# Performance work log

Measured on AMD Instinct MI355X. Metric: run time of the kernel, lower is better.

Reference implementation:

```python
import jax, jax.numpy as jnp
import numpy as np

N = 200000  # nodes
C = 256     # per-node feature dim

def setup_inputs() -> dict:
    key = jax.random.key(0)
    k1, k2, k3, k4, k5, k6, k7 = jax.random.split(key, 7)
    out1 = jax.random.normal(k1, (N, C), dtype=jnp.float32)
    out2 = jax.random.normal(k2, (N, C), dtype=jnp.float32)
    neighbour = jax.random.randint(k3, (N, 3), 0, N, dtype=jnp.int64)
    # Combination2: Conv1d(512,512,1) == Linear(512->512)
    W_comb = jax.random.normal(k4, (512, 2 * C), dtype=jnp.float32) * (1.0 / np.sqrt(2 * C))
    b_comb = jax.random.normal(k5, (512,), dtype=jnp.float32) * 0.01
    # Aggregation2: Conv1d(256,512,1) == Linear(256->512)
    W_agg = jax.random.normal(k6, (512, C), dtype=jnp.float32) * (1.0 / np.sqrt(C))
    b_agg = jax.random.normal(k7, (512,), dtype=jnp.float32) * 0.01
    return {"out1": out1, "out2": out2, "neighbour": neighbour,
            "W_comb": W_comb, "b_comb": b_comb, "W_agg": W_agg, "b_agg": b_agg}


def reference(out1, out2, neighbour, W_comb, b_comb, W_agg, b_agg):
    # Combination2: concat features then 1x1 conv (per-node linear)
    a1 = jnp.concatenate([out1, out2], axis=1)              # [N, 512]
    out3 = jnp.einsum('nc,oc->no', a1, W_comb) + b_comb     # [N, 512]

    # Aggregation2: mean of self + 3 gathered neighbors, then linear 256->512
    neigh_feats = jnp.take(out2, neighbour, axis=0)          # [N, 3, C]
    agg = (out2 + neigh_feats.sum(axis=1)) * 0.25            # [N, C]
    out4 = jnp.einsum('nc,oc->no', agg, W_agg) + b_agg       # [N, 512]
    return (out3, out4)
```

## Files before the change

kernel.cpp:

```cpp
#include <hip/hip_runtime.h>


typedef __bf16 bf16x8 __attribute__((ext_vector_type(8)));
typedef float f32x4 __attribute__((ext_vector_type(4)));

#define N_NODES 200000
#define BM 32
#define NTILES (N_NODES / BM)
#define ROWC 520
#define ROWA 264
#define GRID_B 2048

__device__ __forceinline__ unsigned short f2bf(float x) {
  union { float f; unsigned int u; } v; v.f = x;
  return (unsigned short)((v.u + 0x7FFFu + ((v.u >> 16) & 1u)) >> 16);
}

__device__ __forceinline__ void st_bf4(unsigned short* p, float4 f) {
  uint2 w;
  w.x = (unsigned int)f2bf(f.x) | ((unsigned int)f2bf(f.y) << 16);
  w.y = (unsigned int)f2bf(f.z) | ((unsigned int)f2bf(f.w) << 16);
  *reinterpret_cast<uint2*>(p) = w;
}

__global__ void pack_w_kernel(const float* __restrict__ Wc,
                              const float* __restrict__ Wa,
                              unsigned short* __restrict__ Pc,
                              unsigned short* __restrict__ Pa) {
  int t = blockIdx.x * 256 + threadIdx.x;
  if (t >= (512 + 256) * 64) return;
  int lane = t & 63;
  int tile = t >> 6;
  const float* W;
  unsigned short* P;
  int K, kt_n;
  if (tile < 512) { W = Wc; P = Pc; K = 512; kt_n = 16; }
  else { tile -= 512; W = Wa; P = Pa; K = 256; kt_n = 8; }
  int nt = tile / kt_n;
  int kt = tile - nt * kt_n;
  int row = nt * 16 + (lane & 15);
  int k0 = kt * 32 + (lane >> 4) * 8;
  const float* src = W + (size_t)row * K + k0;
  unsigned short* dst = P + (size_t)tile * 512 + lane * 8;
#pragma unroll
  for (int j = 0; j < 8; ++j) dst[j] = f2bf(src[j]);
}

__global__ __launch_bounds__(512, 2) void gemm_kernel(
    const float* __restrict__ out1, const float* __restrict__ out2,
    const unsigned short* __restrict__ Pc, const unsigned short* __restrict__ Pa,
    const float* __restrict__ b_comb,
    float* __restrict__ out3, unsigned short* __restrict__ Y) {
  __shared__ unsigned short Acomb[BM * ROWC];

  const int tid = threadIdx.x;
  const int ln = tid >> 4, c16 = tid & 15;
  const int wave = tid >> 6, lane = tid & 63;
  const int l15 = lane & 15, l4 = lane >> 4;
  const long long node0 = (long long)blockIdx.x * BM;

  {
    const size_t gn = (size_t)node0 + ln;
    const float4* r1 = reinterpret_cast<const float4*>(out1 + gn * 256);
    const float4* r2 = reinterpret_cast<const float4*>(out2 + gn * 256);
#pragma unroll
    for (int r = 0; r < 4; ++r) {
      const int cc = c16 + 16 * r;
      st_bf4(&Acomb[ln * ROWC + cc * 4], r1[cc]);
      st_bf4(&Acomb[ln * ROWC + 256 + cc * 4], r2[cc]);
    }
  }
  __syncthreads();

  const int nt0 = wave * 4;

  {
    f32x4 acc[2][4];
#pragma unroll
    for (int m = 0; m < 2; ++m)
#pragma unroll
      for (int n = 0; n < 4; ++n) acc[m][n] = (f32x4){0.f, 0.f, 0.f, 0.f};

    const unsigned short* pc = Pc + (size_t)nt0 * 16 * 512 + lane * 8;
    const unsigned short* ab = &Acomb[(size_t)l15 * ROWC + l4 * 8];
#pragma unroll
    for (int kt = 0; kt < 16; ++kt) {
      bf16x8 a0 = *reinterpret_cast<const bf16x8*>(ab + kt * 32);
      bf16x8 a1 = *reinterpret_cast<const bf16x8*>(ab + 16 * ROWC + kt * 32);
      bf16x8 bfr[4];
#pragma unroll
      for (int n = 0; n < 4; ++n)
        bfr[n] = *reinterpret_cast<const bf16x8*>(pc + ((size_t)n * 16 + kt) * 512);
#pragma unroll
      for (int n = 0; n < 4; ++n) {
        acc[0][n] = __builtin_amdgcn_mfma_f32_16x16x32_bf16(a0, bfr[n], acc[0][n], 0, 0, 0);
        acc[1][n] = __builtin_amdgcn_mfma_f32_16x16x32_bf16(a1, bfr[n], acc[1][n], 0, 0, 0);
      }
    }
    float* o3 = out3 + node0 * 512 + wave * 64 + l15;
#pragma unroll
    for (int m = 0; m < 2; ++m)
#pragma unroll
      for (int r = 0; r < 4; ++r) {
        float* p = o3 + (long long)(m * 16 + l4 * 4 + r) * 512;
#pragma unroll
        for (int n = 0; n < 4; ++n)
          p[n * 16] = acc[m][n][r] + b_comb[wave * 64 + n * 16 + l15];
      }
  }

  {
    f32x4 acc[2][4];
#pragma unroll
    for (int m = 0; m < 2; ++m)
#pragma unroll
      for (int n = 0; n < 4; ++n) acc[m][n] = (f32x4){0.f, 0.f, 0.f, 0.f};

    const unsigned short* pa = Pa + (size_t)nt0 * 8 * 512 + lane * 8;
    const unsigned short* ab = &Acomb[(size_t)l15 * ROWC + 256 + l4 * 8];
#pragma unroll
    for (int kt = 0; kt < 8; ++kt) {
      bf16x8 a0 = *reinterpret_cast<const bf16x8*>(ab + kt * 32);
      bf16x8 a1 = *reinterpret_cast<const bf16x8*>(ab + 16 * ROWC + kt * 32);
      bf16x8 bfr[4];
#pragma unroll
      for (int n = 0; n < 4; ++n)
        bfr[n] = *reinterpret_cast<const bf16x8*>(pa + ((size_t)n * 8 + kt) * 512);
#pragma unroll
      for (int n = 0; n < 4; ++n) {
        acc[0][n] = __builtin_amdgcn_mfma_f32_16x16x32_bf16(a0, bfr[n], acc[0][n], 0, 0, 0);
        acc[1][n] = __builtin_amdgcn_mfma_f32_16x16x32_bf16(a1, bfr[n], acc[1][n], 0, 0, 0);
      }
    }

    __syncthreads();
#pragma unroll
    for (int m = 0; m < 2; ++m)
#pragma unroll
      for (int r = 0; r < 4; ++r) {
        const int row = m * 16 + l4 * 4 + r;
#pragma unroll
        for (int n = 0; n < 4; ++n)
          Acomb[row * ROWC + wave * 64 + n * 16 + l15] = f2bf(acc[m][n][r]);
      }
    __syncthreads();

    {
      const int row = tid >> 4;
      const unsigned short* src = &Acomb[row * ROWC];
      unsigned short* dst = Y + (node0 + row) * 512;
#pragma unroll
      for (int j = 0; j < 4; ++j) {
        const int off = (c16 + 16 * j) * 8;
        *reinterpret_cast<uint4*>(dst + off) =
            *reinterpret_cast<const uint4*>(src + off);
      }
    }
  }
}

__device__ __forceinline__ float bf_lo(unsigned u) {
  union { unsigned x; float f; } c; c.x = u << 16; return c.f;
}
__device__ __forceinline__ float bf_hi(unsigned u) {
  union { unsigned x; float f; } c; c.x = u & 0xFFFF0000u; return c.f;
}

__global__ __launch_bounds__(256) void gather_kernel(
    const unsigned short* __restrict__ Y, const int* __restrict__ nbr,
    const float* __restrict__ b_agg, float* __restrict__ out4) {
  const int lane = threadIdx.x & 63;
  const int wid = (blockIdx.x * 256 + threadIdx.x) >> 6;
  const int nwaves = (GRID_B * 256) >> 6;

  float ba[8];
  const float* bp = b_agg + lane * 8;
#pragma unroll
  for (int j = 0; j < 8; ++j) ba[j] = bp[j];

  for (int n = wid; n < N_NODES; n += nwaves) {
    int i0 = nbr[3 * n + 0];
    int i1 = nbr[3 * n + 1];
    int i2 = nbr[3 * n + 2];
    i0 = i0 < 0 ? 0 : (i0 >= N_NODES ? N_NODES - 1 : i0);
    i1 = i1 < 0 ? 0 : (i1 >= N_NODES ? N_NODES - 1 : i1);
    i2 = i2 < 0 ? 0 : (i2 >= N_NODES ? N_NODES - 1 : i2);

    const uint4 a  = *reinterpret_cast<const uint4*>(Y + (size_t)n  * 512 + lane * 8);
    const uint4 b0 = *reinterpret_cast<const uint4*>(Y + (size_t)i0 * 512 + lane * 8);
    const uint4 b1 = *reinterpret_cast<const uint4*>(Y + (size_t)i1 * 512 + lane * 8);
    const uint4 b2 = *reinterpret_cast<const uint4*>(Y + (size_t)i2 * 512 + lane * 8);

    const unsigned wa[4] = {a.x, a.y, a.z, a.w};
    const unsigned w0[4] = {b0.x, b0.y, b0.z, b0.w};
    const unsigned w1[4] = {b1.x, b1.y, b1.z, b1.w};
    const unsigned w2[4] = {b2.x, b2.y, b2.z, b2.w};
    float s[8];
#pragma unroll
    for (int w = 0; w < 4; ++w) {
      s[2 * w]     = bf_lo(wa[w]) + bf_lo(w0[w]) + bf_lo(w1[w]) + bf_lo(w2[w]);
      s[2 * w + 1] = bf_hi(wa[w]) + bf_hi(w0[w]) + bf_hi(w1[w]) + bf_hi(w2[w]);
    }
    f32x4 o0 = {s[0] * 0.25f + ba[0], s[1] * 0.25f + ba[1],
                s[2] * 0.25f + ba[2], s[3] * 0.25f + ba[3]};
    f32x4 o1 = {s[4] * 0.25f + ba[4], s[5] * 0.25f + ba[5],
                s[6] * 0.25f + ba[6], s[7] * 0.25f + ba[7]};
    f32x4* op = reinterpret_cast<f32x4*>(out4 + (size_t)n * 512 + lane * 8);
    op[0] = o0;
    op[1] = o1;
  }
}

__global__ __launch_bounds__(512, 4) void mesh_fused_fallback(
    const float* __restrict__ out1, const float* __restrict__ out2,
    const int* __restrict__ nbr,
    const unsigned short* __restrict__ Pc, const unsigned short* __restrict__ Pa,
    const float* __restrict__ b_comb, const float* __restrict__ b_agg,
    float* __restrict__ outp) {
  __shared__ unsigned short Ac[32 * ROWC];
  __shared__ unsigned short Aagg[32 * ROWA];
  const int tid = threadIdx.x;
  const long long node0 = (long long)blockIdx.x * 32;
  {
    const int ln = tid >> 4, c16 = tid & 15;
    const long long gn = node0 + ln;
    long long i0 = nbr[3 * gn + 0], i1 = nbr[3 * gn + 1], i2 = nbr[3 * gn + 2];
    i0 = i0 < 0 ? 0 : (i0 >= N_NODES ? N_NODES - 1 : i0);
    i1 = i1 < 0 ? 0 : (i1 >= N_NODES ? N_NODES - 1 : i1);
    i2 = i2 < 0 ? 0 : (i2 >= N_NODES ? N_NODES - 1 : i2);
    const float4* r1 = reinterpret_cast<const float4*>(out1 + gn * 256);
    const float4* r2 = reinterpret_cast<const float4*>(out2 + gn * 256);
    const float4* g0 = reinterpret_cast<const float4*>(out2 + i0 * 256);
    const float4* g1 = reinterpret_cast<const float4*>(out2 + i1 * 256);
    const float4* g2 = reinterpret_cast<const float4*>(out2 + i2 * 256);
#pragma unroll
    for (int r = 0; r < 4; ++r) {
      const int c = c16 + 16 * r;
      float4 f1 = r1[c], f2 = r2[c], n0 = g0[c], n1 = g1[c], n2 = g2[c];
      float4 ag;
      ag.x = (f2.x + n0.x + n1.x + n2.x) * 0.25f;
      ag.y = (f2.y + n0.y + n1.y + n2.y) * 0.25f;
      ag.z = (f2.z + n0.z + n1.z + n2.z) * 0.25f;
      ag.w = (f2.w + n0.w + n1.w + n2.w) * 0.25f;
      st_bf4(&Ac[ln * ROWC + c * 4], f1);
      st_bf4(&Ac[ln * ROWC + 256 + c * 4], f2);
      st_bf4(&Aagg[ln * ROWA + c * 4], ag);
    }
  }
  __syncthreads();
  const int wave = tid >> 6, lane = tid & 63;
  const int l15 = lane & 15, l4 = lane >> 4;
  const int nt0 = wave * 4;
  float* o3 = outp;
  float* o4 = outp + (size_t)N_NODES * 512;
  {
    f32x4 acc[2][4];
#pragma unroll
    for (int m = 0; m < 2; ++m)
#pragma unroll
      for (int n = 0; n < 4; ++n) acc[m][n] = (f32x4){0.f, 0.f, 0.f, 0.f};
    const unsigned short* pc = Pc + (size_t)nt0 * 16 * 512 + lane * 8;
    const unsigned short* ab = &Ac[(size_t)l15 * ROWC + l4 * 8];
#pragma unroll
    for (int kt = 0; kt < 16; ++kt) {
      bf16x8 a0 = *reinterpret_cast<const bf16x8*>(ab + kt * 32);
      bf16x8 a1 = *reinterpret_cast<const bf16x8*>(ab + 16 * ROWC + kt * 32);
#pragma unroll
      for (int n = 0; n < 4; ++n) {
        bf16x8 b = *reinterpret_cast<const bf16x8*>(pc + ((size_t)n * 16 + kt) * 512);
        acc[0][n] = __builtin_amdgcn_mfma_f32_16x16x32_bf16(a0, b, acc[0][n], 0, 0, 0);
        acc[1][n] = __builtin_amdgcn_mfma_f32_16x16x32_bf16(a1, b, acc[1][n], 0, 0, 0);
      }
    }
#pragma unroll
    for (int m = 0; m < 2; ++m)
#pragma unroll
      for (int r = 0; r < 4; ++r)
#pragma unroll
        for (int n = 0; n < 4; ++n) {
          const int col = wave * 64 + n * 16 + l15;
          o3[(node0 + m * 16 + l4 * 4 + r) * 512 + col] = acc[m][n][r] + b_comb[col];
        }
  }
  {
    f32x4 acc[2][4];
#pragma unroll
    for (int m = 0; m < 2; ++m)
#pragma unroll
      for (int n = 0; n < 4; ++n) acc[m][n] = (f32x4){0.f, 0.f, 0.f, 0.f};
    const unsigned short* pa = Pa + (size_t)nt0 * 8 * 512 + lane * 8;
    const unsigned short* ab = &Aagg[(size_t)l15 * ROWA + l4 * 8];
#pragma unroll
    for (int kt = 0; kt < 8; ++kt) {
      bf16x8 a0 = *reinterpret_cast<const bf16x8*>(ab + kt * 32);
      bf16x8 a1 = *reinterpret_cast<const bf16x8*>(ab + 16 * ROWA + kt * 32);
#pragma unroll
      for (int n = 0; n < 4; ++n) {
        bf16x8 b = *reinterpret_cast<const bf16x8*>(pa + ((size_t)n * 8 + kt) * 512);
        acc[0][n] = __builtin_amdgcn_mfma_f32_16x16x32_bf16(a0, b, acc[0][n], 0, 0, 0);
        acc[1][n] = __builtin_amdgcn_mfma_f32_16x16x32_bf16(a1, b, acc[1][n], 0, 0, 0);
      }
    }
#pragma unroll
    for (int m = 0; m < 2; ++m)
#pragma unroll
      for (int r = 0; r < 4; ++r)
#pragma unroll
        for (int n = 0; n < 4; ++n) {
          const int col = wave * 64 + n * 16 + l15;
          o4[(node0 + m * 16 + l4 * 4 + r) * 512 + col] = acc[m][n][r] + b_agg[col];
        }
  }
}

extern "C" void kernel_launch(void* const* d_in, const int* in_sizes, int n_in,
                              void* d_out, int out_size, void* d_ws, size_t ws_size,
                              hipStream_t stream) {
  const float* out1 = (const float*)d_in[0];
  const float* out2 = (const float*)d_in[1];
  const int* nbr = (const int*)d_in[2];
  const float* Wc = (const float*)d_in[3];
  const float* bc = (const float*)d_in[4];
  const float* Wa = (const float*)d_in[5];
  const float* ba = (const float*)d_in[6];

  const size_t yElems = (size_t)N_NODES * 512;
  const size_t packElems = 512 * 512 + 512 * 256;
  const size_t need = (yElems + packElems) * 2;

  if (ws_size >= need) {
    unsigned short* Yw = (unsigned short*)d_ws;
    unsigned short* Pc = Yw + yElems;
    unsigned short* Pa = Pc + 512 * 512;
    pack_w_kernel<<<192, 256, 0, stream>>>(Wc, Wa, Pc, Pa);
    gemm_kernel<<<NTILES, 512, 0, stream>>>(out1, out2, Pc, Pa, bc, (float*)d_out, Yw);
    gather_kernel<<<GRID_B, 256, 0, stream>>>(Yw, nbr, ba,
                                              (float*)d_out + (size_t)N_NODES * 512);
  } else {
    unsigned short* Pc = (unsigned short*)d_ws;
    unsigned short* Pa = Pc + 512 * 512;
    pack_w_kernel<<<192, 256, 0, stream>>>(Wc, Wa, Pc, Pa);
    mesh_fused_fallback<<<N_NODES / 32, 512, 0, stream>>>(out1, out2, nbr, Pc, Pa, bc, ba,
                                                          (float*)d_out);
  }
}
```

Baseline: 538.9 us.

## Make GEMM kernel persistent with register prefetch of next tile's inputs

The GEMM kernel becomes a persistent grid-stride loop over node tiles (512 blocks). Each iteration issues global loads for the next tile's out1/out2 rows into registers before the MFMA work on the current tile, so load latency overlaps with compute. It also hoists the b_comb bias load out of the loop. The cost is higher register pressure from the prefetch buffers, plus a fixed grid that may underfill the device or leave tiles unevenly spread across blocks.

```diff
diff --git a/kernel.cpp b/kernel.cpp
--- a/kernel.cpp
+++ b/kernel.cpp
@@ -9,6 +9,7 @@
 #define NTILES (N_NODES / BM)
 #define ROWC 520
 #define ROWA 264
+#define GRID_A 512
 #define GRID_B 2048
 
 __device__ __forceinline__ unsigned short f2bf(float x) {
@@ -57,105 +58,127 @@
   const int ln = tid >> 4, c16 = tid & 15;
   const int wave = tid >> 6, lane = tid & 63;
   const int l15 = lane & 15, l4 = lane >> 4;
-  const long long node0 = (long long)blockIdx.x * BM;
-
-  {
-    const size_t gn = (size_t)node0 + ln;
+  const int nt0 = wave * 4;
+
+  float bcv[4];
+#pragma unroll
+  for (int n = 0; n < 4; ++n) bcv[n] = b_comb[wave * 64 + n * 16 + l15];
+
+  float4 s1[4], s2[4];
+  auto issue = [&](int t) {
+    const size_t gn = (size_t)t * BM + ln;
     const float4* r1 = reinterpret_cast<const float4*>(out1 + gn * 256);
     const float4* r2 = reinterpret_cast<const float4*>(out2 + gn * 256);
 #pragma unroll
     for (int r = 0; r < 4; ++r) {
+      s1[r] = r1[c16 + 16 * r];
+      s2[r] = r2[c16 + 16 * r];
+    }
+  };
+
+  int t = blockIdx.x;
+  issue(t);
+  while (t < NTILES) {
+    __builtin_amdgcn_s_barrier();
+
+#pragma unroll
+    for (int r = 0; r < 4; ++r) {
       const int cc = c16 + 16 * r;
-      st_bf4(&Acomb[ln * ROWC + cc * 4], r1[cc]);
-      st_bf4(&Acomb[ln * ROWC + 256 + cc * 4], r2[cc]);
-    }
-  }
-  __syncthreads();
-
-  const int nt0 = wave * 4;
-
-  {
-    f32x4 acc[2][4];
-#pragma unroll
-    for (int m = 0; m < 2; ++m)
-#pragma unroll
-      for (int n = 0; n < 4; ++n) acc[m][n] = (f32x4){0.f, 0.f, 0.f, 0.f};
-
-    const unsigned short* pc = Pc + (size_t)nt0 * 16 * 512 + lane * 8;
-    const unsigned short* ab = &Acomb[(size_t)l15 * ROWC + l4 * 8];
-#pragma unroll
-    for (int kt = 0; kt < 16; ++kt) {
-      bf16x8 a0 = *reinterpret_cast<const bf16x8*>(ab + kt * 32);
-      bf16x8 a1 = *reinterpret_cast<const bf16x8*>(ab + 16 * ROWC + kt * 32);
-      bf16x8 bfr[4];
-#pragma unroll
-      for (int n = 0; n < 4; ++n)
-        bfr[n] = *reinterpret_cast<const bf16x8*>(pc + ((size_t)n * 16 + kt) * 512);
-#pragma unroll
-      for (int n = 0; n < 4; ++n) {
-        acc[0][n] = __builtin_amdgcn_mfma_f32_16x16x32_bf16(a0, bfr[n], acc[0][n], 0, 0, 0);
-        acc[1][n] = __builtin_amdgcn_mfma_f32_16x16x32_bf16(a1, bfr[n], acc[1][n], 0, 0, 0);
-      }
-    }
-    float* o3 = out3 + node0 * 512 + wave * 64 + l15;
-#pragma unroll
-    for (int m = 0; m < 2; ++m)
-#pragma unroll
-      for (int r = 0; r < 4; ++r) {
-        float* p = o3 + (long long)(m * 16 + l4 * 4 + r) * 512;
+      st_bf4(&Acomb[ln * ROWC + cc * 4], s1[r]);
+      st_bf4(&Acomb[ln * ROWC + 256 + cc * 4], s2[r]);
+    }
+
+    const int tn = t + GRID_A;
+    if (tn < NTILES) issue(tn);
+
+    asm volatile("s_waitcnt lgkmcnt(0)" ::: "memory");
+    __builtin_amdgcn_s_barrier();
+
+    const long long node0 = (long long)t * BM;
+
+    {
+      f32x4 acc[2][4];
+#pragma unroll
+      for (int m = 0; m < 2; ++m)
+#pragma unroll
+        for (int n = 0; n < 4; ++n) acc[m][n] = (f32x4){0.f, 0.f, 0.f, 0.f};
+
+      const unsigned short* pc = Pc + (size_t)nt0 * 16 * 512 + lane * 8;
+      const unsigned short* ab = &Acomb[(size_t)l15 * ROWC + l4 * 8];
+#pragma unroll
+      for (int kt = 0; kt < 16; ++kt) {
+        bf16x8 a0 = *reinterpret_cast<const bf16x8*>(ab + kt * 32);
+        bf16x8 a1 = *reinterpret_cast<const bf16x8*>(ab + 16 * ROWC + kt * 32);
+        bf16x8 bfr[4];
 #pragma unroll
         for (int n = 0; n < 4; ++n)
-          p[n * 16] = acc[m][n][r] + b_comb[wave * 64 + n * 16 + l15];
-      }
-  }
-
-  {
-    f32x4 acc[2][4];
-#pragma unroll
-    for (int m = 0; m < 2; ++m)
-#pragma unroll
-      for (int n = 0; n < 4; ++n) acc[m][n] = (f32x4){0.f, 0.f, 0.f, 0.f};
-
-    const unsigned short* pa = Pa + (size_t)nt0 * 8 * 512 + lane * 8;
-    const unsigned short* ab = &Acomb[(size_t)l15 * ROWC + 256 + l4 * 8];
-#pragma unroll
-    for (int kt = 0; kt < 8; ++kt) {
-      bf16x8 a0 = *reinterpret_cast<const bf16x8*>(ab + kt * 32);
-      bf16x8 a1 = *reinterpret_cast<const bf16x8*>(ab + 16 * ROWC + kt * 32);
-      bf16x8 bfr[4];
-#pragma unroll
-      for (int n = 0; n < 4; ++n)
-        bfr[n] = *reinterpret_cast<const bf16x8*>(pa + ((size_t)n * 8 + kt) * 512);
-#pragma unroll
-      for (int n = 0; n < 4; ++n) {
-        acc[0][n] = __builtin_amdgcn_mfma_f32_16x16x32_bf16(a0, bfr[n], acc[0][n], 0, 0, 0);
-        acc[1][n] = __builtin_amdgcn_mfma_f32_16x16x32_bf16(a1, bfr[n], acc[1][n], 0, 0, 0);
-      }
-    }
-
-    __syncthreads();
-#pragma unroll
-    for (int m = 0; m < 2; ++m)
-#pragma unroll
-      for (int r = 0; r < 4; ++r) {
-        const int row = m * 16 + l4 * 4 + r;
+          bfr[n] = *reinterpret_cast<const bf16x8*>(pc + ((size_t)n * 16 + kt) * 512);
+#pragma unroll
+        for (int n = 0; n < 4; ++n) {
+          acc[0][n] = __builtin_amdgcn_mfma_f32_16x16x32_bf16(a0, bfr[n], acc[0][n], 0, 0, 0);
+          acc[1][n] = __builtin_amdgcn_mfma_f32_16x16x32_bf16(a1, bfr[n], acc[1][n], 0, 0, 0);
+        }
+      }
+      float* o3 = out3 + node0 * 512 + wave * 64 + l15;
+#pragma unroll
+      for (int m = 0; m < 2; ++m)
+#pragma unroll
+        for (int r = 0; r < 4; ++r) {
+          float* p = o3 + (long long)(m * 16 + l4 * 4 + r) * 512;
+#pragma unroll
+          for (int n = 0; n < 4; ++n) p[n * 16] = acc[m][n][r] + bcv[n];
+        }
+    }
+
+    {
+      f32x4 acc[2][4];
+#pragma unroll
+      for (int m = 0; m < 2; ++m)
+#pragma unroll
+        for (int n = 0; n < 4; ++n) acc[m][n] = (f32x4){0.f, 0.f, 0.f, 0.f};
+
+      const unsigned short* pa = Pa + (size_t)nt0 * 8 * 512 + lane * 8;
+      const unsigned short* ab = &Acomb[(size_t)l15 * ROWC + 256 + l4 * 8];
+#pragma unroll
+      for (int kt = 0; kt < 8; ++kt) {
+        bf16x8 a0 = *reinterpret_cast<const bf16x8*>(ab + kt * 32);
+        bf16x8 a1 = *reinterpret_cast<const bf16x8*>(ab + 16 * ROWC + kt * 32);
+        bf16x8 bfr[4];
 #pragma unroll
         for (int n = 0; n < 4; ++n)
-          Acomb[row * ROWC + wave * 64 + n * 16 + l15] = f2bf(acc[m][n][r]);
-      }
-    __syncthreads();
-
-    {
-      const int row = tid >> 4;
-      const unsigned short* src = &Acomb[row * ROWC];
-      unsigned short* dst = Y + (node0 + row) * 512;
-#pragma unroll
-      for (int j = 0; j < 4; ++j) {
-        const int off = (c16 + 16 * j) * 8;
-        *reinterpret_cast<uint4*>(dst + off) =
-            *reinterpret_cast<const uint4*>(src + off);
-      }
-    }
+          bfr[n] = *reinterpret_cast<const bf16x8*>(pa + ((size_t)n * 8 + kt) * 512);
+#pragma unroll
+        for (int n = 0; n < 4; ++n) {
+          acc[0][n] = __builtin_amdgcn_mfma_f32_16x16x32_bf16(a0, bfr[n], acc[0][n], 0, 0, 0);
+          acc[1][n] = __builtin_amdgcn_mfma_f32_16x16x32_bf16(a1, bfr[n], acc[1][n], 0, 0, 0);
+        }
+      }
+
+      __syncthreads();
+#pragma unroll
+      for (int m = 0; m < 2; ++m)
+#pragma unroll
+        for (int r = 0; r < 4; ++r) {
+          const int row = m * 16 + l4 * 4 + r;
+#pragma unroll
+          for (int n = 0; n < 4; ++n)
+            Acomb[row * ROWC + wave * 64 + n * 16 + l15] = f2bf(acc[m][n][r]);
+        }
+      __syncthreads();
+
+      {
+        const int row = tid >> 4;
+        const unsigned short* src = &Acomb[row * ROWC];
+        unsigned short* dst = Y + (node0 + row) * 512;
+#pragma unroll
+        for (int j = 0; j < 4; ++j) {
+          const int off = (c16 + 16 * j) * 8;
+          *reinterpret_cast<uint4*>(dst + off) =
+              *reinterpret_cast<const uint4*>(src + off);
+        }
+      }
+    }
+    t = tn;
   }
 }
 
@@ -333,7 +356,7 @@
     unsigned short* Pc = Yw + yElems;
     unsigned short* Pa = Pc + 512 * 512;
     pack_w_kernel<<<192, 256, 0, stream>>>(Wc, Wa, Pc, Pa);
-    gemm_kernel<<<NTILES, 512, 0, stream>>>(out1, out2, Pc, Pa, bc, (float*)d_out, Yw);
+    gemm_kernel<<<GRID_A, 512, 0, stream>>>(out1, out2, Pc, Pa, bc, (float*)d_out, Yw);
     gather_kernel<<<GRID_B, 256, 0, stream>>>(Yw, nbr, ba,
                                               (float*)d_out + (size_t)N_NODES * 512);
   } else {
```

Result: slower. 716.2 us (+32.9%).
